# Performance work log

Hardware: AMD Instinct MI355X
Metric: run time of the kernel (lower is better)

The kernel has to match this reference:

```python
import jax, jax.numpy as jnp
import numpy as np

DIMENSIONS = 10000
NUM_LEVELS = 100
SIZE = 617
NUM_CLASSES = 26
BATCH = 32


def setup_inputs() -> dict:
    key = jax.random.key(0)
    k1, k2, k3 = jax.random.split(key, 3)
    x = jax.random.uniform(k1, (BATCH, SIZE), dtype=jnp.float32)  # values in [0,1]
    # Random embedding: bipolar {-1,+1} hypervectors
    id_weight = jnp.where(jax.random.uniform(k2, (SIZE, DIMENSIONS)) > 0.5, 1.0, -1.0).astype(jnp.float32)
    # Level embedding: bipolar hypervectors per quantization level
    level_weight = jnp.where(jax.random.uniform(k3, (NUM_LEVELS, DIMENSIONS)) > 0.5, 1.0, -1.0).astype(jnp.float32)
    classify_weight = jnp.zeros((NUM_CLASSES, DIMENSIONS), dtype=jnp.float32)
    return {"x": x, "id_weight": id_weight, "level_weight": level_weight, "classify_weight": classify_weight}


def reference(x, id_weight, level_weight, classify_weight):
    # Level embedding: map continuous values in [low=0, high=1] to level indices
    idx = jnp.clip(jnp.round(x * (NUM_LEVELS - 1)), 0, NUM_LEVELS - 1).astype(jnp.int32)  # (B, S)
    value_hv = level_weight[idx]                     # gather -> (B, S, D)
    bound = id_weight[None, :, :] * value_hv         # bind (elementwise multiply)
    multiset = jnp.sum(bound, axis=1)                # sum over feature axis -> (B, D)
    enc = jnp.where(multiset > 0, 1.0, -1.0)         # hard_quantize
    logit = jnp.einsum('bd,cd->bc', enc, classify_weight)  # Linear, no bias
    return logit
```

## Files before the change

### kernel.cpp

```cpp
#include <hip/hip_runtime.h>

typedef unsigned int u32;
typedef unsigned char u8;
typedef unsigned long long u64;

#define DIMS   10000
#define LEVELS 100
#define SSIZE  617
#define SPAD   624
#define NCLS   26
#define BATCH  32
#define WORDS  313
#define WPITCH 320
#define DPITCH 10240
#define NTILE  5
#define NCH    26
#define CHUNK  24

#define OFF_OFFB 0x000000u
#define OFF_IDB  0x020000u
#define OFF_LVB  0x100000u
#define OFF_P8   0x140000u
#define SLOT_BYTES ((size_t)BATCH * DPITCH)

#define PK_ROWS (SPAD + LEVELS)

__global__ __launch_bounds__(256) void k_pack(const float* __restrict__ x,
                                              const float* __restrict__ idw,
                                              const float* __restrict__ lvw,
                                              u32* __restrict__ idb,
                                              u32* __restrict__ lvb,
                                              u32* __restrict__ offb,
                                              float* __restrict__ out)
{
    const int g = blockIdx.x;
    const int r = blockIdx.y;
    const int t = threadIdx.x;
    const bool isLvl = r >= SPAD;
    const int d0 = g * 1024 + 4 * t;

    u32 nib = 0;
    if (d0 + 3 < DIMS && (isLvl || r < SSIZE)) {
        const float* src = isLvl ? (lvw + (size_t)(r - SPAD) * DIMS)
                                 : (idw + (size_t)r * DIMS);
        float4 f = *(const float4*)(src + d0);
        nib =  (__builtin_bit_cast(u32, f.x) >> 31)
            | ((__builtin_bit_cast(u32, f.y) >> 31) << 1)
            | ((__builtin_bit_cast(u32, f.z) >> 31) << 2)
            | ((__builtin_bit_cast(u32, f.w) >> 31) << 3);
    }
    __shared__ u32 nibs[256];
    nibs[t] = nib;
    __syncthreads();
    if (t < 32) {
        u32 w = 0;
#pragma unroll
        for (int j = 0; j < 8; ++j) w |= nibs[t * 8 + j] << (4 * j);
        u32* dst = isLvl ? (lvb + (size_t)(r - SPAD) * WPITCH)
                         : (idb + (size_t)r * WPITCH);
        dst[g * 32 + t] = w;
    }

    const int B = r * 10 + g;
    const int t2 = B * 256 + t;
    if (t2 < SPAD * BATCH) {
        int s = t2 >> 5, b = t2 & 31;
        u32 off = LEVELS * 256u;
        if (s < SSIZE) {
            float v = x[b * SSIZE + s];
            float rr = rintf(v * (float)(LEVELS - 1));
            int q = (int)rr;
            q = q < 0 ? 0 : (q > LEVELS - 1 ? LEVELS - 1 : q);
            off = (u32)q * 256u;
        }
        offb[s * BATCH + b] = off;
    }
    if (t2 < BATCH * NCLS) out[t2] = 0.0f;
}

__device__ __forceinline__ void spread_store(u32* __restrict__ part,
                                             int slot, int B0, int wq,
                                             const u32 ones[8], const u32 c0[8],
                                             const u32 c1[8], const u32 c2[8],
                                             const u32 c3[8], const u32 c4[8])
{
#pragma unroll
    for (int b = 0; b < 8; ++b) {
        u32* dst = part + ((size_t)(slot * BATCH + B0 + b) * DPITCH + (size_t)wq * 32) / 4;
        u32 o[8];
#pragma unroll
        for (int g = 0; g < 8; ++g) {
            int sh = 4 * g;
            u32 n;
            n  =  (((ones[b] >> sh) & 0xFu) * 0x00204081u) & 0x01010101u;
            n |= ((((c0[b]  >> sh) & 0xFu) * 0x00204081u) & 0x01010101u) << 1;
            n |= ((((c1[b]  >> sh) & 0xFu) * 0x00204081u) & 0x01010101u) << 2;
            n |= ((((c2[b]  >> sh) & 0xFu) * 0x00204081u) & 0x01010101u) << 3;
            n |= ((((c3[b]  >> sh) & 0xFu) * 0x00204081u) & 0x01010101u) << 4;
            n |= ((((c4[b]  >> sh) & 0xFu) * 0x00204081u) & 0x01010101u) << 5;
            o[g] = n;
        }
        *(uint4*)(dst)     = make_uint4(o[0], o[1], o[2], o[3]);
        *(uint4*)(dst + 4) = make_uint4(o[4], o[5], o[6], o[7]);
    }
}

#define CSA_STEP(b, x1, x2)                                                   \
    {                                                                         \
        u32 t0 = (x1) ^ (x2);                                                 \
        u32 sum = ones[b] ^ t0;                                               \
        u32 car = ((x1) & (x2)) | (ones[b] & t0);                             \
        ones[b] = sum;                                                        \
        u32 tt;                                                               \
        tt = c0[b] & car; c0[b] ^= car; car = tt;                             \
        tt = c1[b] & car; c1[b] ^= car; car = tt;                             \
        tt = c2[b] & car; c2[b] ^= car; car = tt;                             \
        tt = c3[b] & car; c3[b] ^= car; car = tt;                             \
        c4[b] ^= car;                                                         \
    }

template <int CH>
__global__ __launch_bounds__(256) void k_bind_t(const u32* __restrict__ idb,
                                                const u32* __restrict__ lvb,
                                                const u32* __restrict__ offb,
                                                u32* __restrict__ part)
{
    __shared__ u32 tile[(LEVELS + 1) * 64];
    const int W0 = blockIdx.x * 64;
    const int slot = blockIdx.y;
    const int tid = threadIdx.x;

    {
        u32 stg[25];
#pragma unroll
        for (int k = 0; k < 25; ++k) {
            int idx = k * 256 + tid;
            stg[k] = lvb[(size_t)(idx >> 6) * WPITCH + W0 + (idx & 63)];
        }
#pragma unroll
        for (int k = 0; k < 25; ++k) tile[k * 256 + tid] = stg[k];
        if (tid < 64) tile[6400 + tid] = 0;
    }
    __syncthreads();

    const int lane = tid & 63;
    const int B0 = __builtin_amdgcn_readfirstlane((tid >> 6) * 8);
    const int wq = W0 + lane;
    const int sBeg = slot * CH;

    u32 ones[8], c0[8], c1[8], c2[8], c3[8], c4[8];
#pragma unroll
    for (int b = 0; b < 8; ++b) { ones[b]=0; c0[b]=0; c1[b]=0; c2[b]=0; c3[b]=0; c4[b]=0; }

#pragma unroll
    for (int i = 0; i < CH / 2; ++i) {
        const int s = sBeg + 2 * i;
        u32 u1 = idb[(size_t)s * WPITCH + wq];
        u32 u2 = idb[(size_t)(s + 1) * WPITCH + wq];
        const u32* o1 = offb + s * BATCH + B0;
        const u32* o2 = o1 + BATCH;
#pragma unroll
        for (int b = 0; b < 8; ++b) {
            u32 l1 = tile[(o1[b] >> 2) + lane];
            u32 l2 = tile[(o2[b] >> 2) + lane];
            u32 x1 = u1 ^ l1, x2 = u2 ^ l2;
            CSA_STEP(b, x1, x2);
        }
    }
    spread_store(part, slot, B0, wq, ones, c0, c1, c2, c3, c4);
}

__global__ __launch_bounds__(256) void k_bind_g(const u32* __restrict__ idb,
                                                const u32* __restrict__ lvb,
                                                const u32* __restrict__ offb,
                                                u32* __restrict__ part,
                                                int chunk)
{
    __shared__ u32 tile[(LEVELS + 1) * 64];
    const int W0 = blockIdx.x * 64;
    const int slot = blockIdx.y;
    const int tid = threadIdx.x;
    for (int t = tid; t < (LEVELS + 1) * 64; t += 256) {
        int r = t >> 6, w = t & 63;
        tile[t] = (r < LEVELS) ? lvb[(size_t)r * WPITCH + W0 + w] : 0;
    }
    __syncthreads();
    const int lane = tid & 63;
    const int B0 = __builtin_amdgcn_readfirstlane((tid >> 6) * 8);
    const int wq = W0 + lane;
    const int sBeg = slot * chunk;
    const int sEnd = min(SPAD, sBeg + chunk);
    u32 ones[8], c0[8], c1[8], c2[8], c3[8], c4[8];
#pragma unroll
    for (int b = 0; b < 8; ++b) { ones[b]=0; c0[b]=0; c1[b]=0; c2[b]=0; c3[b]=0; c4[b]=0; }
    for (int s = sBeg; s < sEnd; s += 2) {
        u32 u1 = idb[(size_t)s * WPITCH + wq];
        u32 u2 = idb[(size_t)(s + 1) * WPITCH + wq];
        const u32* o1 = offb + s * BATCH + B0;
        const u32* o2 = o1 + BATCH;
#pragma unroll
        for (int b = 0; b < 8; ++b) {
            u32 l1 = tile[(o1[b] >> 2) + lane];
            u32 l2 = tile[(o2[b] >> 2) + lane];
            u32 x1 = u1 ^ l1, x2 = u2 ^ l2;
            CSA_STEP(b, x1, x2);
        }
    }
    spread_store(part, slot, B0, wq, ones, c0, c1, c2, c3, c4);
}

template <int NCHT>
__global__ __launch_bounds__(256) void k_encl_t(const u32* __restrict__ part,
                                                const float* __restrict__ W,
                                                float* __restrict__ out)
{
    const int b = blockIdx.y;
    const int q = blockIdx.x;
    const int t = threadIdx.x;
    const int dw = q * 256 + t;
    const u32* p = part + (size_t)b * (DPITCH / 4) + dw;
    const size_t cs = (size_t)BATCH * (DPITCH / 4);

    u32 v[NCHT];
#pragma unroll
    for (int c = 0; c < NCHT; ++c) v[c] = p[(size_t)c * cs];
    u32 a01 = 0, a23 = 0;
#pragma unroll
    for (int c = 0; c < NCHT; ++c) {
        a01 += v[c] & 0x00FF00FFu;
        a23 += (v[c] >> 8) & 0x00FF00FFu;
    }
    const float e0 = (int)(a01 & 0xFFFFu) <= 308 ? 1.0f : -1.0f;
    const float e1 = (int)(a23 & 0xFFFFu) <= 308 ? 1.0f : -1.0f;
    const float e2 = (int)(a01 >> 16)     <= 308 ? 1.0f : -1.0f;
    const float e3 = (int)(a23 >> 16)     <= 308 ? 1.0f : -1.0f;

    float acc[NCLS];
    if (dw < DIMS / 4) {
#pragma unroll
        for (int cc = 0; cc < NCLS; ++cc) {
            float4 w4 = *(const float4*)(W + (size_t)cc * DIMS + 4 * dw);
            acc[cc] = fmaf(e0, w4.x, fmaf(e1, w4.y, fmaf(e2, w4.z, e3 * w4.w)));
        }
    } else {
#pragma unroll
        for (int cc = 0; cc < NCLS; ++cc) acc[cc] = 0.0f;
    }

#pragma unroll
    for (int cc = 0; cc < NCLS; ++cc) {
#pragma unroll
        for (int o = 32; o > 0; o >>= 1)
            acc[cc] += __shfl_xor(acc[cc], o);
    }
    __shared__ float red[4][NCLS];
    const int lane = t & 63, wv = t >> 6;
    if (lane == 0) {
#pragma unroll
        for (int cc = 0; cc < NCLS; ++cc) red[wv][cc] = acc[cc];
    }
    __syncthreads();
    if (t < NCLS) {
        float vv = red[0][t] + red[1][t] + red[2][t] + red[3][t];
        atomicAdd(out + b * NCLS + t, vv);
    }
}

__global__ __launch_bounds__(256) void k_encl_g(const u32* __restrict__ part,
                                                const float* __restrict__ W,
                                                float* __restrict__ out,
                                                int nch)
{
    const int b = blockIdx.y;
    const int q = blockIdx.x;
    const int t = threadIdx.x;
    const int dw = q * 256 + t;
    const u32* p = part + (size_t)b * (DPITCH / 4) + dw;
    const size_t cs = (size_t)BATCH * (DPITCH / 4);
    u32 a01 = 0, a23 = 0;
    for (int c = 0; c < nch; ++c) {
        u32 v = p[(size_t)c * cs];
        a01 += v & 0x00FF00FFu;
        a23 += (v >> 8) & 0x00FF00FFu;
    }
    const float e0 = (int)(a01 & 0xFFFFu) <= 308 ? 1.0f : -1.0f;
    const float e1 = (int)(a23 & 0xFFFFu) <= 308 ? 1.0f : -1.0f;
    const float e2 = (int)(a01 >> 16)     <= 308 ? 1.0f : -1.0f;
    const float e3 = (int)(a23 >> 16)     <= 308 ? 1.0f : -1.0f;
    float acc[NCLS];
    if (dw < DIMS / 4) {
#pragma unroll
        for (int cc = 0; cc < NCLS; ++cc) {
            float4 w4 = *(const float4*)(W + (size_t)cc * DIMS + 4 * dw);
            acc[cc] = fmaf(e0, w4.x, fmaf(e1, w4.y, fmaf(e2, w4.z, e3 * w4.w)));
        }
    } else {
#pragma unroll
        for (int cc = 0; cc < NCLS; ++cc) acc[cc] = 0.0f;
    }
#pragma unroll
    for (int cc = 0; cc < NCLS; ++cc) {
#pragma unroll
        for (int o = 32; o > 0; o >>= 1)
            acc[cc] += __shfl_xor(acc[cc], o);
    }
    __shared__ float red[4][NCLS];
    const int lane = t & 63, wv = t >> 6;
    if (lane == 0) {
#pragma unroll
        for (int cc = 0; cc < NCLS; ++cc) red[wv][cc] = acc[cc];
    }
    __syncthreads();
    if (t < NCLS) {
        float vv = red[0][t] + red[1][t] + red[2][t] + red[3][t];
        atomicAdd(out + b * NCLS + t, vv);
    }
}

extern "C" void kernel_launch(void* const* d_in, const int* in_sizes, int n_in,
                              void* d_out, int out_size, void* d_ws, size_t ws_size,
                              hipStream_t stream)
{
    const float* x   = (const float*)d_in[0];
    const float* idw = (const float*)d_in[1];
    const float* lvw = (const float*)d_in[2];
    const float* W   = (const float*)d_in[3];
    float* out = (float*)d_out;

    char* ws = (char*)d_ws;
    u32* offb = (u32*)(ws + OFF_OFFB);
    u32* idb  = (u32*)(ws + OFF_IDB);
    u32* lvb  = (u32*)(ws + OFF_LVB);
    u32* part = (u32*)(ws + OFF_P8);

    size_t avail = ws_size > OFF_P8 ? ws_size - OFF_P8 : 0;
    const bool fast = avail >= (size_t)NCH * SLOT_BYTES;

    dim3 g1(10, PK_ROWS);
    k_pack<<<g1, 256, 0, stream>>>(x, idw, lvw, idb, lvb, offb, out);

    if (fast) {
        dim3 g2(NTILE, NCH);
        k_bind_t<CHUNK><<<g2, 256, 0, stream>>>(idb, lvb, offb, part);
        dim3 g3(10, BATCH);
        k_encl_t<NCH><<<g3, 256, 0, stream>>>(part, W, out);
    } else {
        int nch = (int)(avail / SLOT_BYTES);
        if (nch < 1) nch = 1;
        int chunk = (SPAD + nch - 1) / nch;
        chunk = (chunk + 1) & ~1;
        if (chunk > 62) chunk = 62;
        nch = (SPAD + chunk - 1) / chunk;
        dim3 g2(NTILE, nch);
        k_bind_g<<<g2, 256, 0, stream>>>(idb, lvb, offb, part, chunk);
        dim3 g3(10, BATCH);
        k_encl_g<<<g3, 256, 0, stream>>>(part, W, out, nch);
    }
}
```

Measured before the change: 100.1 us.

## Drop LDS level tile; read level words from global with single-wave blocks

The bind kernels no longer stage the level-hypervector tile in shared memory. Each lane gathers level words straight from global memory (L1/L2 cached), using word offsets of q*WPITCH, with a zero row for padding supplied by an extra pack row. The grid is now split over batch groups of 4 with 64-thread blocks, and the fast path drops one carry plane because a 24-row chunk fits in 5 bits. This gives about eight times more small blocks and removes the LDS fill and barrier. In exchange, the level table is read through cache gathers rather than LDS, and idb words are reloaded once per batch group.

```diff
diff --git a/kernel.cpp b/kernel.cpp
--- a/kernel.cpp
+++ b/kernel.cpp
@@ -17,31 +17,33 @@
 #define NCH    26
 #define CHUNK  24
 
-#define OFF_OFFB 0x000000u
+#define OFF_OFFW 0x000000u
 #define OFF_IDB  0x020000u
 #define OFF_LVB  0x100000u
 #define OFF_P8   0x140000u
 #define SLOT_BYTES ((size_t)BATCH * DPITCH)
 
-#define PK_ROWS (SPAD + LEVELS)
+#define PK_ROWS (SPAD + LEVELS + 1)
 
 __global__ __launch_bounds__(256) void k_pack(const float* __restrict__ x,
                                               const float* __restrict__ idw,
                                               const float* __restrict__ lvw,
                                               u32* __restrict__ idb,
                                               u32* __restrict__ lvb,
-                                              u32* __restrict__ offb,
+                                              u32* __restrict__ offw,
                                               float* __restrict__ out)
 {
     const int g = blockIdx.x;
     const int r = blockIdx.y;
     const int t = threadIdx.x;
     const bool isLvl = r >= SPAD;
+    const int rl = r - SPAD;
     const int d0 = g * 1024 + 4 * t;
 
     u32 nib = 0;
-    if (d0 + 3 < DIMS && (isLvl || r < SSIZE)) {
-        const float* src = isLvl ? (lvw + (size_t)(r - SPAD) * DIMS)
+    const bool rowValid = isLvl ? (rl < LEVELS) : (r < SSIZE);
+    if (d0 + 3 < DIMS && rowValid) {
+        const float* src = isLvl ? (lvw + (size_t)rl * DIMS)
                                  : (idw + (size_t)r * DIMS);
         float4 f = *(const float4*)(src + d0);
         nib =  (__builtin_bit_cast(u32, f.x) >> 31)
@@ -56,7 +58,7 @@
         u32 w = 0;
 #pragma unroll
         for (int j = 0; j < 8; ++j) w |= nibs[t * 8 + j] << (4 * j);
-        u32* dst = isLvl ? (lvb + (size_t)(r - SPAD) * WPITCH)
+        u32* dst = isLvl ? (lvb + (size_t)rl * WPITCH)
                          : (idb + (size_t)r * WPITCH);
         dst[g * 32 + t] = w;
     }
@@ -65,27 +67,118 @@
     const int t2 = B * 256 + t;
     if (t2 < SPAD * BATCH) {
         int s = t2 >> 5, b = t2 & 31;
-        u32 off = LEVELS * 256u;
+        u32 off = (u32)LEVELS * WPITCH;
         if (s < SSIZE) {
             float v = x[b * SSIZE + s];
             float rr = rintf(v * (float)(LEVELS - 1));
             int q = (int)rr;
             q = q < 0 ? 0 : (q > LEVELS - 1 ? LEVELS - 1 : q);
-            off = (u32)q * 256u;
-        }
-        offb[s * BATCH + b] = off;
+            off = (u32)q * WPITCH;
+        }
+        offw[s * BATCH + b] = off;
     }
     if (t2 < BATCH * NCLS) out[t2] = 0.0f;
 }
 
-__device__ __forceinline__ void spread_store(u32* __restrict__ part,
-                                             int slot, int B0, int wq,
-                                             const u32 ones[8], const u32 c0[8],
-                                             const u32 c1[8], const u32 c2[8],
-                                             const u32 c3[8], const u32 c4[8])
-{
-#pragma unroll
-    for (int b = 0; b < 8; ++b) {
+template <int CH>
+__global__ __launch_bounds__(64) void k_bind_t(const u32* __restrict__ idb,
+                                               const u32* __restrict__ lvb,
+                                               const u32* __restrict__ offw,
+                                               u32* __restrict__ part)
+{
+    const int wq   = blockIdx.x * 64 + threadIdx.x;
+    const int B0   = blockIdx.y * 4;
+    const int slot = blockIdx.z;
+    const int sBeg = slot * CH;
+
+    u32 ones[4], c0[4], c1[4], c2[4], c3[4];
+#pragma unroll
+    for (int b = 0; b < 4; ++b) { ones[b]=0; c0[b]=0; c1[b]=0; c2[b]=0; c3[b]=0; }
+
+#pragma unroll
+    for (int i = 0; i < CH / 2; ++i) {
+        const int s = sBeg + 2 * i;
+        u32 u1 = idb[(size_t)s * WPITCH + wq];
+        u32 u2 = idb[(size_t)(s + 1) * WPITCH + wq];
+        const u32* o1 = offw + s * BATCH + B0;
+        const u32* o2 = o1 + BATCH;
+#pragma unroll
+        for (int b = 0; b < 4; ++b) {
+            u32 l1 = lvb[o1[b] + wq];
+            u32 l2 = lvb[o2[b] + wq];
+            u32 x1 = u1 ^ l1, x2 = u2 ^ l2;
+            u32 t0 = x1 ^ x2;
+            u32 sum = ones[b] ^ t0;
+            u32 car = (x1 & x2) | (ones[b] & t0);
+            ones[b] = sum;
+            u32 tt;
+            tt = c0[b] & car; c0[b] ^= car; car = tt;
+            tt = c1[b] & car; c1[b] ^= car; car = tt;
+            tt = c2[b] & car; c2[b] ^= car; car = tt;
+            c3[b] ^= car;
+        }
+    }
+
+#pragma unroll
+    for (int b = 0; b < 4; ++b) {
+        u32* dst = part + ((size_t)(slot * BATCH + B0 + b) * DPITCH + (size_t)wq * 32) / 4;
+        u32 o[8];
+#pragma unroll
+        for (int g = 0; g < 8; ++g) {
+            int sh = 4 * g;
+            u32 n;
+            n  =  (((ones[b] >> sh) & 0xFu) * 0x00204081u) & 0x01010101u;
+            n |= ((((c0[b]  >> sh) & 0xFu) * 0x00204081u) & 0x01010101u) << 1;
+            n |= ((((c1[b]  >> sh) & 0xFu) * 0x00204081u) & 0x01010101u) << 2;
+            n |= ((((c2[b]  >> sh) & 0xFu) * 0x00204081u) & 0x01010101u) << 3;
+            n |= ((((c3[b]  >> sh) & 0xFu) * 0x00204081u) & 0x01010101u) << 4;
+            o[g] = n;
+        }
+        *(uint4*)(dst)     = make_uint4(o[0], o[1], o[2], o[3]);
+        *(uint4*)(dst + 4) = make_uint4(o[4], o[5], o[6], o[7]);
+    }
+}
+
+__global__ __launch_bounds__(64) void k_bind_g(const u32* __restrict__ idb,
+                                               const u32* __restrict__ lvb,
+                                               const u32* __restrict__ offw,
+                                               u32* __restrict__ part,
+                                               int chunk)
+{
+    const int wq   = blockIdx.x * 64 + threadIdx.x;
+    const int B0   = blockIdx.y * 4;
+    const int slot = blockIdx.z;
+    const int sBeg = slot * chunk;
+    const int sEnd = min(SPAD, sBeg + chunk);
+
+    u32 ones[4], c0[4], c1[4], c2[4], c3[4], c4[4];
+#pragma unroll
+    for (int b = 0; b < 4; ++b) { ones[b]=0; c0[b]=0; c1[b]=0; c2[b]=0; c3[b]=0; c4[b]=0; }
+
+    for (int s = sBeg; s < sEnd; s += 2) {
+        u32 u1 = idb[(size_t)s * WPITCH + wq];
+        u32 u2 = idb[(size_t)(s + 1) * WPITCH + wq];
+        const u32* o1 = offw + s * BATCH + B0;
+        const u32* o2 = o1 + BATCH;
+#pragma unroll
+        for (int b = 0; b < 4; ++b) {
+            u32 l1 = lvb[o1[b] + wq];
+            u32 l2 = lvb[o2[b] + wq];
+            u32 x1 = u1 ^ l1, x2 = u2 ^ l2;
+            u32 t0 = x1 ^ x2;
+            u32 sum = ones[b] ^ t0;
+            u32 car = (x1 & x2) | (ones[b] & t0);
+            ones[b] = sum;
+            u32 tt;
+            tt = c0[b] & car; c0[b] ^= car; car = tt;
+            tt = c1[b] & car; c1[b] ^= car; car = tt;
+            tt = c2[b] & car; c2[b] ^= car; car = tt;
+            tt = c3[b] & car; c3[b] ^= car; car = tt;
+            c4[b] ^= car;
+        }
+    }
+#pragma unroll
+    for (int b = 0; b < 4; ++b) {
         u32* dst = part + ((size_t)(slot * BATCH + B0 + b) * DPITCH + (size_t)wq * 32) / 4;
         u32 o[8];
 #pragma unroll
@@ -103,110 +196,6 @@
         *(uint4*)(dst)     = make_uint4(o[0], o[1], o[2], o[3]);
         *(uint4*)(dst + 4) = make_uint4(o[4], o[5], o[6], o[7]);
     }
-}
-
-#define CSA_STEP(b, x1, x2)                                                   \
-    {                                                                         \
-        u32 t0 = (x1) ^ (x2);                                                 \
-        u32 sum = ones[b] ^ t0;                                               \
-        u32 car = ((x1) & (x2)) | (ones[b] & t0);                             \
-        ones[b] = sum;                                                        \
-        u32 tt;                                                               \
-        tt = c0[b] & car; c0[b] ^= car; car = tt;                             \
-        tt = c1[b] & car; c1[b] ^= car; car = tt;                             \
-        tt = c2[b] & car; c2[b] ^= car; car = tt;                             \
-        tt = c3[b] & car; c3[b] ^= car; car = tt;                             \
-        c4[b] ^= car;                                                         \
-    }
-
-template <int CH>
-__global__ __launch_bounds__(256) void k_bind_t(const u32* __restrict__ idb,
-                                                const u32* __restrict__ lvb,
-                                                const u32* __restrict__ offb,
-                                                u32* __restrict__ part)
-{
-    __shared__ u32 tile[(LEVELS + 1) * 64];
-    const int W0 = blockIdx.x * 64;
-    const int slot = blockIdx.y;
-    const int tid = threadIdx.x;
-
-    {
-        u32 stg[25];
-#pragma unroll
-        for (int k = 0; k < 25; ++k) {
-            int idx = k * 256 + tid;
-            stg[k] = lvb[(size_t)(idx >> 6) * WPITCH + W0 + (idx & 63)];
-        }
-#pragma unroll
-        for (int k = 0; k < 25; ++k) tile[k * 256 + tid] = stg[k];
-        if (tid < 64) tile[6400 + tid] = 0;
-    }
-    __syncthreads();
-
-    const int lane = tid & 63;
-    const int B0 = __builtin_amdgcn_readfirstlane((tid >> 6) * 8);
-    const int wq = W0 + lane;
-    const int sBeg = slot * CH;
-
-    u32 ones[8], c0[8], c1[8], c2[8], c3[8], c4[8];
-#pragma unroll
-    for (int b = 0; b < 8; ++b) { ones[b]=0; c0[b]=0; c1[b]=0; c2[b]=0; c3[b]=0; c4[b]=0; }
-
-#pragma unroll
-    for (int i = 0; i < CH / 2; ++i) {
-        const int s = sBeg + 2 * i;
-        u32 u1 = idb[(size_t)s * WPITCH + wq];
-        u32 u2 = idb[(size_t)(s + 1) * WPITCH + wq];
-        const u32* o1 = offb + s * BATCH + B0;
-        const u32* o2 = o1 + BATCH;
-#pragma unroll
-        for (int b = 0; b < 8; ++b) {
-            u32 l1 = tile[(o1[b] >> 2) + lane];
-            u32 l2 = tile[(o2[b] >> 2) + lane];
-            u32 x1 = u1 ^ l1, x2 = u2 ^ l2;
-            CSA_STEP(b, x1, x2);
-        }
-    }
-    spread_store(part, slot, B0, wq, ones, c0, c1, c2, c3, c4);
-}
-
-__global__ __launch_bounds__(256) void k_bind_g(const u32* __restrict__ idb,
-                                                const u32* __restrict__ lvb,
-                                                const u32* __restrict__ offb,
-                                                u32* __restrict__ part,
-                                                int chunk)
-{
-    __shared__ u32 tile[(LEVELS + 1) * 64];
-    const int W0 = blockIdx.x * 64;
-    const int slot = blockIdx.y;
-    const int tid = threadIdx.x;
-    for (int t = tid; t < (LEVELS + 1) * 64; t += 256) {
-        int r = t >> 6, w = t & 63;
-        tile[t] = (r < LEVELS) ? lvb[(size_t)r * WPITCH + W0 + w] : 0;
-    }
-    __syncthreads();
-    const int lane = tid & 63;
-    const int B0 = __builtin_amdgcn_readfirstlane((tid >> 6) * 8);
-    const int wq = W0 + lane;
-    const int sBeg = slot * chunk;
-    const int sEnd = min(SPAD, sBeg + chunk);
-    u32 ones[8], c0[8], c1[8], c2[8], c3[8], c4[8];
-#pragma unroll
-    for (int b = 0; b < 8; ++b) { ones[b]=0; c0[b]=0; c1[b]=0; c2[b]=0; c3[b]=0; c4[b]=0; }
-    for (int s = sBeg; s < sEnd; s += 2) {
-        u32 u1 = idb[(size_t)s * WPITCH + wq];
-        u32 u2 = idb[(size_t)(s + 1) * WPITCH + wq];
-        const u32* o1 = offb + s * BATCH + B0;
-        const u32* o2 = o1 + BATCH;
-#pragma unroll
-        for (int b = 0; b < 8; ++b) {
-            u32 l1 = tile[(o1[b] >> 2) + lane];
-            u32 l2 = tile[(o2[b] >> 2) + lane];
-            u32 x1 = u1 ^ l1, x2 = u2 ^ l2;
-            CSA_STEP(b, x1, x2);
-        }
-    }
-    spread_store(part, slot, B0, wq, ones, c0, c1, c2, c3, c4);
 }
 
 template <int NCHT>
@@ -328,7 +317,7 @@
     float* out = (float*)d_out;
 
     char* ws = (char*)d_ws;
-    u32* offb = (u32*)(ws + OFF_OFFB);
+    u32* offw = (u32*)(ws + OFF_OFFW);
     u32* idb  = (u32*)(ws + OFF_IDB);
     u32* lvb  = (u32*)(ws + OFF_LVB);
     u32* part = (u32*)(ws + OFF_P8);
@@ -337,11 +326,11 @@
     const bool fast = avail >= (size_t)NCH * SLOT_BYTES;
 
     dim3 g1(10, PK_ROWS);
-    k_pack<<<g1, 256, 0, stream>>>(x, idw, lvw, idb, lvb, offb, out);
+    k_pack<<<g1, 256, 0, stream>>>(x, idw, lvw, idb, lvb, offw, out);
 
     if (fast) {
-        dim3 g2(NTILE, NCH);
-        k_bind_t<CHUNK><<<g2, 256, 0, stream>>>(idb, lvb, offb, part);
+        dim3 g2(NTILE, 8, NCH);
+        k_bind_t<CHUNK><<<g2, 64, 0, stream>>>(idb, lvb, offw, part);
         dim3 g3(10, BATCH);
         k_encl_t<NCH><<<g3, 256, 0, stream>>>(part, W, out);
     } else {
@@ -351,8 +340,8 @@
         chunk = (chunk + 1) & ~1;
         if (chunk > 62) chunk = 62;
         nch = (SPAD + chunk - 1) / chunk;
-        dim3 g2(NTILE, nch);
-        k_bind_g<<<g2, 256, 0, stream>>>(idb, lvb, offb, part, chunk);
+        dim3 g2(NTILE, 8, nch);
+        k_bind_g<<<g2, 64, 0, stream>>>(idb, lvb, offw, part, chunk);
         dim3 g3(10, BATCH);
         k_encl_g<<<g3, 256, 0, stream>>>(part, W, out, nch);
     }
```

Result: faster. 95.24 us (-4.9%).
